# Performance work log

Hardware: AMD Instinct MI355X
Metric: run time of the kernel (lower is better)

Reference implementation:

```python
import jax, jax.numpy as jnp
import numpy as np

# Model dims (see init_kwargs): embed_dim=64, heads=8, d_k = n_wires = 8
V, D, H, NQ, L, FFN = 32000, 64, 8, 8, 2, 128
B, S = 16, 1024
LAT, H1, H2, NC = 32, 128, 64, 10
INV_SQRT_DK = 1.0 / float(np.sqrt(NQ))
LN_EPS = 1e-5


def _pos_encoding(s, d):
    pos = jnp.arange(s, dtype=jnp.float32)[:, None]
    div = jnp.exp(jnp.arange(0, d, 2, dtype=jnp.float32) * (-np.log(10000.0) / d))
    pe = jnp.zeros((s, d), dtype=jnp.float32)
    pe = pe.at[:, 0::2].set(jnp.sin(pos * div))
    pe = pe.at[:, 1::2].set(jnp.cos(pos * div))
    return pe


def _layernorm(x, g, b):
    mu = jnp.mean(x, axis=-1, keepdims=True)
    var = jnp.mean(jnp.square(x - mu), axis=-1, keepdims=True)
    return (x - mu) * jax.lax.rsqrt(var + LN_EPS) * g + b


def _quantum_heads(x, theta):
    # Analytic simulation of the per-head 8-qubit VQC:
    #   RX(x_i) RX(theta_i) on wire i, CNOT ring (0->1..6->7, 7->0), measure Z.
    # Heisenberg picture: <Z_j> = prod_{i=0..j} cos(x_i+theta_i) for j>=1,
    # <Z_0> = prod_{i=1..7} cos(x_i+theta_i).
    b, s, _ = x.shape
    a = x.reshape(b, s, H, NQ) + theta            # [B,S,H,NQ]
    c = jnp.cos(a)
    cp = jnp.cumprod(c, axis=-1)
    z0 = jnp.prod(c[..., 1:], axis=-1, keepdims=True)
    return jnp.concatenate([z0, cp[..., 1:]], axis=-1)  # [B,S,H,NQ]


def _quantum_attention(x, theta, combine_W):
    qkv = _quantum_heads(x, theta)                 # [B,S,H,dk]
    q = qkv.transpose(0, 2, 1, 3)                  # [B,H,S,dk]
    scores = jnp.einsum('bhqd,bhkd->bhqk', q, q) * INV_SQRT_DK
    p = jax.nn.softmax(scores, axis=-1)
    out = jnp.einsum('bhqk,bhkd->bhqd', p, q)
    out = out.transpose(0, 2, 1, 3).reshape(x.shape[0], x.shape[1], D)
    return out @ combine_W.T                       # no bias (use_bias=False)


def _quantum_ffn(x, theta, W1, b1, W2, b2):
    # FFN QLayer: RX(x_i) then RY(theta_i), no entanglement -> <Z_i> = cos(theta_i)*cos(x_i)
    # GeneralEncoder only reads the first NQ features of each token.
    z = jnp.cos(x[..., :NQ]) * jnp.cos(theta)      # [B,S,NQ]
    h = jax.nn.relu(z @ W1.T + b1)                 # linear1 then ReLU
    return h @ W2.T + b2                           # linear2


def _forward(tokens, emb_table, attn_theta, combine_W, ln1_g, ln1_b, ln2_g, ln2_b,
             ffn_theta, ffn_W1, ffn_b1, ffn_W2, ffn_b2,
             enc_W1, enc_b1, enc_W2, enc_b2, enc_W3, enc_b3,
             dec_W1, dec_b1, dec_W2, dec_b2, dec_W3, dec_b3, cls_W, cls_b):
    x = emb_table[tokens] + _pos_encoding(tokens.shape[1], D)  # embed + positional
    for l in range(L):  # fixed small number of structurally distinct blocks
        a = _quantum_attention(x, attn_theta[l], combine_W[l])
        x = _layernorm(x + a, ln1_g[l], ln1_b[l])
        f = _quantum_ffn(x, ffn_theta[l], ffn_W1[l], ffn_b1[l], ffn_W2[l], ffn_b2[l])
        x = _layernorm(x + f, ln2_g[l], ln2_b[l])
    pooled = jnp.mean(x, axis=1)                   # [B,D]
    # AutoencoderQuantumNet.forward = decode(encode(x)) (quantum_ffn unused there)
    h = jax.nn.relu(pooled @ enc_W1.T + enc_b1)
    h = jax.nn.relu(h @ enc_W2.T + enc_b2)
    lat = h @ enc_W3.T + enc_b3
    h = jax.nn.relu(lat @ dec_W1.T + dec_b1)
    h = jax.nn.relu(h @ dec_W2.T + dec_b2)
    rec = h @ dec_W3.T + dec_b3                    # [B,D]
    return rec @ cls_W.T + cls_b                   # [B,NC]


def setup_inputs() -> dict:
    key = jax.random.key(0)
    ks = list(jax.random.split(key, 32))
    it = iter(ks)
    def nrm(shape, scale=0.05):
        return (jax.random.normal(next(it), shape) * scale).astype(jnp.float32)
    return {
        'tokens': jax.random.randint(next(it), (B, S), 0, V),
        'emb_table': nrm((V, D), 0.02),
        'attn_theta': nrm((L, NQ), 0.1),
        'combine_W': nrm((L, D, D)),
        'ln1_g': jnp.ones((L, D), jnp.float32), 'ln1_b': jnp.zeros((L, D), jnp.float32),
        'ln2_g': jnp.ones((L, D), jnp.float32), 'ln2_b': jnp.zeros((L, D), jnp.float32),
        'ffn_theta': nrm((L, NQ), 0.1),
        'ffn_W1': nrm((L, FFN, NQ)), 'ffn_b1': jnp.zeros((L, FFN), jnp.float32),
        'ffn_W2': nrm((L, D, FFN)), 'ffn_b2': jnp.zeros((L, D), jnp.float32),
        'enc_W1': nrm((H1, D)), 'enc_b1': jnp.zeros((H1,), jnp.float32),
        'enc_W2': nrm((H2, H1)), 'enc_b2': jnp.zeros((H2,), jnp.float32),
        'enc_W3': nrm((LAT, H2)), 'enc_b3': jnp.zeros((LAT,), jnp.float32),
        'dec_W1': nrm((H2, LAT)), 'dec_b1': jnp.zeros((H2,), jnp.float32),
        'dec_W2': nrm((H1, H2)), 'dec_b2': jnp.zeros((H1,), jnp.float32),
        'dec_W3': nrm((D, H1)), 'dec_b3': jnp.zeros((D,), jnp.float32),
        'cls_W': nrm((NC, D)), 'cls_b': jnp.zeros((NC,), jnp.float32),
    }


def reference(tokens, emb_table, attn_theta, combine_W, ln1_g, ln1_b, ln2_g, ln2_b,
              ffn_theta, ffn_W1, ffn_b1, ffn_W2, ffn_b2,
              enc_W1, enc_b1, enc_W2, enc_b2, enc_W3, enc_b3,
              dec_W1, dec_b1, dec_W2, dec_b2, dec_W3, dec_b3, cls_W, cls_b):
    return _forward(tokens, emb_table, attn_theta, combine_W, ln1_g, ln1_b, ln2_g, ln2_b,
                    ffn_theta, ffn_W1, ffn_b1, ffn_W2, ffn_b2,
                    enc_W1, enc_b1, enc_W2, enc_b2, enc_W3, enc_b3,
                    dec_W1, dec_b1, dec_W2, dec_b2, dec_W3, dec_b3, cls_W, cls_b)
```

## Files before the change

kernel.cpp:

```cpp
#include <hip/hip_runtime.h>
#include <math.h>

typedef _Float16 h2 __attribute__((ext_vector_type(2)));
typedef __fp16 hh4 __attribute__((ext_vector_type(4)));
typedef float f4 __attribute__((ext_vector_type(4)));

#define Bsz 16
#define Ssz 1024
#define TOKENS (Bsz * Ssz)
#define Dd 64
#define Hh 8
#define QTTS 520

#if __has_builtin(__builtin_amdgcn_exp2f)
  #define EXPFN(x) __builtin_amdgcn_exp2f(x)
  #define SQRT_PRESCALE 0.7141921f
#else
  #define EXPFN(x) __expf(x)
  #define SQRT_PRESCALE 0.5946036f
#endif

#if __has_builtin(__builtin_amdgcn_mfma_f32_16x16x16_f16)
  #define MFMA16(a, b, c) __builtin_amdgcn_mfma_f32_16x16x16_f16(a, b, c, 0, 0, 0)
#else
  #define MFMA16(a, b, c) __builtin_amdgcn_mfma_f32_16x16x16f16(a, b, c, 0, 0, 0)
#endif

__device__ __forceinline__ h2 pkrtz(float a, float b) {
#if __has_builtin(__builtin_amdgcn_cvt_pkrtz)
  return __builtin_bit_cast(h2, __builtin_amdgcn_cvt_pkrtz(a, b));
#else
  h2 r; r.x = (_Float16)a; r.y = (_Float16)b; return r;
#endif
}
__device__ __forceinline__ unsigned int as_u32(h2 v) {
  return __builtin_bit_cast(unsigned int, v);
}
__device__ __forceinline__ hh4 bc4(uint2 u) {
  return __builtin_bit_cast(hh4, u);
}

__device__ __forceinline__ void qheads(const float* __restrict__ xp,
                                       const float* th, float* o) {
  float4 v0 = *(const float4*)(xp);
  float4 v1 = *(const float4*)(xp + 4);
  float c0 = __cosf(v0.x + th[0]), c1 = __cosf(v0.y + th[1]);
  float c2 = __cosf(v0.z + th[2]), c3 = __cosf(v0.w + th[3]);
  float c4 = __cosf(v1.x + th[4]), c5 = __cosf(v1.y + th[5]);
  float c6 = __cosf(v1.z + th[6]), c7 = __cosf(v1.w + th[7]);
  float cp = c0;
  cp *= c1; o[1] = cp; cp *= c2; o[2] = cp; cp *= c3; o[3] = cp;
  cp *= c4; o[4] = cp; cp *= c5; o[5] = cp; cp *= c6; o[6] = cp;
  cp *= c7; o[7] = cp;
  o[0] = c1 * c2 * c3 * c4 * c5 * c6 * c7;
}

__global__ __launch_bounds__(256) void embed_kernel(
    const int* __restrict__ tokens, const float* __restrict__ emb,
    float* __restrict__ x) {
  int gid = blockIdx.x * 256 + threadIdx.x;
  if (gid >= TOKENS * 32) return;
  int d2 = gid & 31;
  int ts = gid >> 5;
  int s  = ts & (Ssz - 1);
  int tok = tokens[ts];
  float freq = __expf((float)(2 * d2) * (-0.14391156831f));
  float ang = (float)s * freq;
  float sn, cs;
  __sincosf(ang, &sn, &cs);
  float2 e2 = *(const float2*)&emb[(size_t)tok * Dd + 2 * d2];
  float2 r;
  r.x = e2.x + sn;
  r.y = e2.y + cs;
  *(float2*)&x[(size_t)ts * Dd + 2 * d2] = r;
}

__global__ __launch_bounds__(256, 4) void attn_kernel(
    const float* __restrict__ x, const float* __restrict__ theta,
    float* __restrict__ o_out, float* __restrict__ ps_out) {
  __shared__ unsigned int qrs[Ssz * 4 + 2];
  __shared__ unsigned int qtt[9 * QTTS];
  int blk = blockIdx.x;
  int bh = blk >> 3, split = blk & 7;
  int b = bh >> 3, h = bh & 7;
  int t = threadIdx.x;

  float th[8];
#pragma unroll
  for (int i = 0; i < 8; i++) th[i] = theta[i];

  const float* xb = x + (size_t)b * Ssz * Dd + h * 8;

#pragma unroll
  for (int i = 0; i < 4; i += 2) {
    int k0 = t * 4 + i;
    float oa[8], ob[8];
    qheads(xb + (size_t)k0 * Dd, th, oa);
    qheads(xb + (size_t)(k0 + 1) * Dd, th, ob);
    uint4 wa, wb;
    wa.x = as_u32(pkrtz(oa[0] * SQRT_PRESCALE, oa[1] * SQRT_PRESCALE));
    wa.y = as_u32(pkrtz(oa[2] * SQRT_PRESCALE, oa[3] * SQRT_PRESCALE));
    wa.z = as_u32(pkrtz(oa[4] * SQRT_PRESCALE, oa[5] * SQRT_PRESCALE));
    wa.w = as_u32(pkrtz(oa[6] * SQRT_PRESCALE, oa[7] * SQRT_PRESCALE));
    wb.x = as_u32(pkrtz(ob[0] * SQRT_PRESCALE, ob[1] * SQRT_PRESCALE));
    wb.y = as_u32(pkrtz(ob[2] * SQRT_PRESCALE, ob[3] * SQRT_PRESCALE));
    wb.z = as_u32(pkrtz(ob[4] * SQRT_PRESCALE, ob[5] * SQRT_PRESCALE));
    wb.w = as_u32(pkrtz(ob[6] * SQRT_PRESCALE, ob[7] * SQRT_PRESCALE));
    *(uint4*)&qrs[k0 * 4] = wa;
    *(uint4*)&qrs[(k0 + 1) * 4] = wb;
#pragma unroll
    for (int d = 0; d < 8; d++)
      qtt[d * QTTS + (k0 >> 1)] = as_u32(pkrtz(oa[d], ob[d]));
  }
  for (int j = 8 * QTTS + t; j < 9 * QTTS; j += 256) qtt[j] = 0x3C003C00u;
  if (t == 0) { qrs[Ssz * 4] = 0; qrs[Ssz * 4 + 1] = 0; }
  __syncthreads();

  int l = t & 63, w = t >> 6;
  int g = l >> 4, rr = l & 15;
  int rt0 = split * 8 + w * 2;
  int rowA = rt0 * 16 + rr;
  int rowB = rowA + 16;
  uint2 z2; z2.x = 0; z2.y = 0;
  uint2 buA = (g < 2) ? *(const uint2*)&qrs[rowA * 4 + 2 * g] : z2;
  uint2 buB = (g < 2) ? *(const uint2*)&qrs[rowB * 4 + 2 * g] : z2;
  hh4 BrA = bc4(buA), BrB = bc4(buB);
  int aoff  = (g < 2) ? (rr * 4 + 2 * g) : (Ssz * 4);
  int astep = (g < 2) ? 64 : 0;
  int qrow  = (rr >= 8) ? 8 : rr;
  int qoff  = qrow * QTTS + 2 * g;
  f4 zf = {0.f, 0.f, 0.f, 0.f};
  f4 accA0 = zf, accB0 = zf, accA1 = zf, accB1 = zf;

#pragma unroll 4
  for (int kt = 0; kt < 64; kt += 2) {
    {
      uint2 au = *(const uint2*)&qrs[aoff + kt * astep];
      hh4 Ak = bc4(au);
      f4 sA = MFMA16(Ak, BrA, zf);
      f4 sB = MFMA16(Ak, BrB, zf);
      float pA0 = EXPFN(sA.x), pA1 = EXPFN(sA.y), pA2 = EXPFN(sA.z), pA3 = EXPFN(sA.w);
      float pB0 = EXPFN(sB.x), pB1 = EXPFN(sB.y), pB2 = EXPFN(sB.z), pB3 = EXPFN(sB.w);
      uint2 pbA, pbB;
      pbA.x = as_u32(pkrtz(pA0, pA1)); pbA.y = as_u32(pkrtz(pA2, pA3));
      pbB.x = as_u32(pkrtz(pB0, pB1)); pbB.y = as_u32(pkrtz(pB2, pB3));
      uint2 qt = *(const uint2*)&qtt[qoff + kt * 8];
      hh4 Aq = bc4(qt);
      accA0 = MFMA16(Aq, bc4(pbA), accA0);
      accB0 = MFMA16(Aq, bc4(pbB), accB0);
    }
    {
      uint2 au = *(const uint2*)&qrs[aoff + (kt + 1) * astep];
      hh4 Ak = bc4(au);
      f4 sA = MFMA16(Ak, BrA, zf);
      f4 sB = MFMA16(Ak, BrB, zf);
      float pA0 = EXPFN(sA.x), pA1 = EXPFN(sA.y), pA2 = EXPFN(sA.z), pA3 = EXPFN(sA.w);
      float pB0 = EXPFN(sB.x), pB1 = EXPFN(sB.y), pB2 = EXPFN(sB.z), pB3 = EXPFN(sB.w);
      uint2 pbA, pbB;
      pbA.x = as_u32(pkrtz(pA0, pA1)); pbA.y = as_u32(pkrtz(pA2, pA3));
      pbB.x = as_u32(pkrtz(pB0, pB1)); pbB.y = as_u32(pkrtz(pB2, pB3));
      uint2 qt = *(const uint2*)&qtt[qoff + (kt + 1) * 8];
      hh4 Aq = bc4(qt);
      accA1 = MFMA16(Aq, bc4(pbA), accA1);
      accB1 = MFMA16(Aq, bc4(pbB), accB1);
    }
  }
  f4 accA = accA0 + accA1;
  f4 accB = accB0 + accB1;

  size_t tokA = (size_t)b * Ssz + rowA;
  size_t tokB = (size_t)b * Ssz + rowB;
  if (g < 2) {
    *(f4*)&o_out[tokA * 64 + h * 8 + 4 * g] = accA;
    *(f4*)&o_out[tokB * 64 + h * 8 + 4 * g] = accB;
  } else if (g == 2) {
    ps_out[tokA * 8 + h] = accA.x;
    ps_out[tokB * 8 + h] = accB.x;
  }
}

__global__ __launch_bounds__(64) void tail_kernel(
    float* __restrict__ x, const float* __restrict__ o_out,
    const float* __restrict__ ps_out, const float* __restrict__ Wc,
    const float* __restrict__ g1, const float* __restrict__ bb1,
    const float* __restrict__ g2, const float* __restrict__ bb2,
    const float* __restrict__ fth,
    const float* __restrict__ W1, const float* __restrict__ fb1,
    const float* __restrict__ W2, const float* __restrict__ fb2,
    float* __restrict__ partial, int do_partial) {
  __shared__ float xbuf[16][68];
  int l = threadIdx.x & 63;
  int g = l >> 4, c = l & 15;
  int tok0 = blockIdx.x * 16;
  f4 zf = {0.f, 0.f, 0.f, 0.f};

  {
    hh4 Bf[4][4];
#pragma unroll
    for (int dc = 0; dc < 4; dc++)
#pragma unroll
      for (int kc = 0; kc < 4; kc++) {
        float4 wv = *(const float4*)&Wc[(size_t)(dc * 16 + c) * 64 + kc * 16 + 4 * g];
        uint2 u; u.x = as_u32(pkrtz(wv.x, wv.y)); u.y = as_u32(pkrtz(wv.z, wv.w));
        Bf[kc][dc] = bc4(u);
      }
    int tka = tok0 + c;
    hh4 Af[4];
#pragma unroll
    for (int kc = 0; kc < 4; kc++) {
      float4 o4 = *(const float4*)&o_out[(size_t)tka * 64 + kc * 16 + 4 * g];
      float inv = 1.0f / ps_out[(size_t)tka * 8 + kc * 2 + (g >> 1)];
      uint2 u;
      u.x = as_u32(pkrtz(o4.x * inv, o4.y * inv));
      u.y = as_u32(pkrtz(o4.z * inv, o4.w * inv));
      Af[kc] = bc4(u);
    }
    float yy[4][4];
#pragma unroll
    for (int dc = 0; dc < 4; dc++) {
      f4 acc = zf;
#pragma unroll
      for (int kc = 0; kc < 4; kc++) acc = MFMA16(Af[kc], Bf[kc][dc], acc);
      yy[dc][0] = acc.x; yy[dc][1] = acc.y; yy[dc][2] = acc.z; yy[dc][3] = acc.w;
    }
    float g1v[4], b1v[4];
#pragma unroll
    for (int dc = 0; dc < 4; dc++) { g1v[dc] = g1[dc * 16 + c]; b1v[dc] = bb1[dc * 16 + c]; }
#pragma unroll
    for (int r = 0; r < 4; r++) {
      int tok = tok0 + 4 * g + r;
      float rv0 = x[(size_t)tok * 64 + c]      + yy[0][r];
      float rv1 = x[(size_t)tok * 64 + 16 + c] + yy[1][r];
      float rv2 = x[(size_t)tok * 64 + 32 + c] + yy[2][r];
      float rv3 = x[(size_t)tok * 64 + 48 + c] + yy[3][r];
      float s = (rv0 + rv1) + (rv2 + rv3);
      s += __shfl_xor(s, 1, 64); s += __shfl_xor(s, 2, 64);
      s += __shfl_xor(s, 4, 64); s += __shfl_xor(s, 8, 64);
      float mu = s * (1.f / 64.f);
      float t0 = rv0 - mu, t1 = rv1 - mu, t2 = rv2 - mu, t3 = rv3 - mu;
      float q = (t0 * t0 + t1 * t1) + (t2 * t2 + t3 * t3);
      q += __shfl_xor(q, 1, 64); q += __shfl_xor(q, 2, 64);
      q += __shfl_xor(q, 4, 64); q += __shfl_xor(q, 8, 64);
      float inv = rsqrtf(q * (1.f / 64.f) + 1e-5f);
      int tk = 4 * g + r;
      xbuf[tk][c]      = t0 * inv * g1v[0] + b1v[0];
      xbuf[tk][16 + c] = t1 * inv * g1v[1] + b1v[1];
      xbuf[tk][32 + c] = t2 * inv * g1v[2] + b1v[2];
      xbuf[tk][48 + c] = t3 * inv * g1v[3] + b1v[3];
    }
  }

  float4 x4[4];
#pragma unroll
  for (int dc = 0; dc < 4; dc++)
    x4[dc] = *(const float4*)&xbuf[c][dc * 16 + 4 * g];

  uint2 uz; uz.x = 0; uz.y = 0;
  if (g < 2) {
    float4 thv = *(const float4*)&fth[4 * g];
    float z0 = __cosf(x4[0].x) * __cosf(thv.x);
    float z1 = __cosf(x4[0].y) * __cosf(thv.y);
    float z2 = __cosf(x4[0].z) * __cosf(thv.z);
    float z3 = __cosf(x4[0].w) * __cosf(thv.w);
    uz.x = as_u32(pkrtz(z0, z1)); uz.y = as_u32(pkrtz(z2, z3));
  }
  hh4 Bz = bc4(uz);

  hh4 Bh[8];
#pragma unroll
  for (int jc = 0; jc < 8; jc++) {
    uint2 uw; uw.x = 0; uw.y = 0;
    if (g < 2) {
      float4 wv = *(const float4*)&W1[(size_t)(jc * 16 + c) * 8 + 4 * g];
      uw.x = as_u32(pkrtz(wv.x, wv.y)); uw.y = as_u32(pkrtz(wv.z, wv.w));
    }
    f4 d1 = MFMA16(bc4(uw), Bz, zf);
    float4 b1v = *(const float4*)&fb1[jc * 16 + 4 * g];
    float h0 = fmaxf(d1.x + b1v.x, 0.f);
    float h1 = fmaxf(d1.y + b1v.y, 0.f);
    float h2 = fmaxf(d1.z + b1v.z, 0.f);
    float h3 = fmaxf(d1.w + b1v.w, 0.f);
    uint2 uh;
    uh.x = as_u32(pkrtz(h0, h1)); uh.y = as_u32(pkrtz(h2, h3));
    Bh[jc] = bc4(uh);
  }

  float ff[4][4];
#pragma unroll
  for (int dc = 0; dc < 4; dc++) {
    f4 acc = zf;
#pragma unroll
    for (int kc = 0; kc < 8; kc++) {
      float4 wv = *(const float4*)&W2[(size_t)(dc * 16 + c) * 128 + kc * 16 + 4 * g];
      uint2 uw;
      uw.x = as_u32(pkrtz(wv.x, wv.y)); uw.y = as_u32(pkrtz(wv.z, wv.w));
      acc = MFMA16(bc4(uw), Bh[kc], acc);
    }
    ff[dc][0] = acc.x; ff[dc][1] = acc.y; ff[dc][2] = acc.z; ff[dc][3] = acc.w;
  }

  float r2[4][4];
  float s = 0.f;
#pragma unroll
  for (int dc = 0; dc < 4; dc++) {
    float4 b2v = *(const float4*)&fb2[dc * 16 + 4 * g];
    r2[dc][0] = x4[dc].x + ff[dc][0] + b2v.x;
    r2[dc][1] = x4[dc].y + ff[dc][1] + b2v.y;
    r2[dc][2] = x4[dc].z + ff[dc][2] + b2v.z;
    r2[dc][3] = x4[dc].w + ff[dc][3] + b2v.w;
    s += (r2[dc][0] + r2[dc][1]) + (r2[dc][2] + r2[dc][3]);
  }
  s += __shfl_xor(s, 16, 64); s += __shfl_xor(s, 32, 64);
  float mu = s * (1.f / 64.f);
  float q = 0.f;
#pragma unroll
  for (int dc = 0; dc < 4; dc++) {
#pragma unroll
    for (int r = 0; r < 4; r++) { r2[dc][r] -= mu; q += r2[dc][r] * r2[dc][r]; }
  }
  q += __shfl_xor(q, 16, 64); q += __shfl_xor(q, 32, 64);
  float inv = rsqrtf(q * (1.f / 64.f) + 1e-5f);

  float xo[4][4];
#pragma unroll
  for (int dc = 0; dc < 4; dc++) {
    float4 gv = *(const float4*)&g2[dc * 16 + 4 * g];
    float4 bv = *(const float4*)&bb2[dc * 16 + 4 * g];
    xo[dc][0] = r2[dc][0] * inv * gv.x + bv.x;
    xo[dc][1] = r2[dc][1] * inv * gv.y + bv.y;
    xo[dc][2] = r2[dc][2] * inv * gv.z + bv.z;
    xo[dc][3] = r2[dc][3] * inv * gv.w + bv.w;
    float4 o4;
    o4.x = xo[dc][0]; o4.y = xo[dc][1]; o4.z = xo[dc][2]; o4.w = xo[dc][3];
    *(float4*)&x[(size_t)(tok0 + c) * 64 + dc * 16 + 4 * g] = o4;
  }

  if (do_partial) {
#pragma unroll
    for (int dc = 0; dc < 4; dc++)
#pragma unroll
      for (int r = 0; r < 4; r++) {
        float p = xo[dc][r];
        p += __shfl_xor(p, 1, 64); p += __shfl_xor(p, 2, 64);
        p += __shfl_xor(p, 4, 64); p += __shfl_xor(p, 8, 64);
        xo[dc][r] = p;
      }
    if (c == 0) {
#pragma unroll
      for (int dc = 0; dc < 4; dc++) {
        float4 o4;
        o4.x = xo[dc][0]; o4.y = xo[dc][1]; o4.z = xo[dc][2]; o4.w = xo[dc][3];
        *(float4*)&partial[(size_t)blockIdx.x * 64 + dc * 16 + 4 * g] = o4;
      }
    }
  }
}

__global__ __launch_bounds__(128) void head_kernel(
    const float* __restrict__ partial,
    const float* eW1, const float* eb1, const float* eW2, const float* eb2,
    const float* eW3, const float* eb3, const float* dW1, const float* db1v,
    const float* dW2, const float* db2v, const float* dW3, const float* db3v,
    const float* cW, const float* cb, float* __restrict__ out) {
  __shared__ float bufP[64];
  __shared__ float bufA[128];
  __shared__ float bufB[128];
  int b = blockIdx.x, t = threadIdx.x;
  if (t < 64) {
    float s = 0.f;
    for (int c = 0; c < 64; ++c) s += partial[(size_t)(b * 64 + c) * 64 + t];
    bufP[t] = s * (1.f / 1024.f);
  }
  __syncthreads();
  {
    float v = eb1[t];
    for (int d = 0; d < 64; d++) v = fmaf(bufP[d], eW1[t * 64 + d], v);
    bufA[t] = fmaxf(v, 0.f);
  }
  __syncthreads();
  if (t < 64) {
    float v = eb2[t];
    for (int j = 0; j < 128; j++) v = fmaf(bufA[j], eW2[t * 128 + j], v);
    bufB[t] = fmaxf(v, 0.f);
  }
  __syncthreads();
  if (t < 32) {
    float v = eb3[t];
    for (int d = 0; d < 64; d++) v = fmaf(bufB[d], eW3[t * 64 + d], v);
    bufA[t] = v;
  }
  __syncthreads();
  if (t < 64) {
    float v = db1v[t];
    for (int k = 0; k < 32; k++) v = fmaf(bufA[k], dW1[t * 32 + k], v);
    bufB[t] = fmaxf(v, 0.f);
  }
  __syncthreads();
  {
    float v = db2v[t];
    for (int k = 0; k < 64; k++) v = fmaf(bufB[k], dW2[t * 64 + k], v);
    bufA[t] = fmaxf(v, 0.f);
  }
  __syncthreads();
  if (t < 64) {
    float v = db3v[t];
    for (int j = 0; j < 128; j++) v = fmaf(bufA[j], dW3[t * 128 + j], v);
    bufB[t] = v;
  }
  __syncthreads();
  if (t < 10) {
    float v = cb[t];
    for (int d = 0; d < 64; d++) v = fmaf(bufB[d], cW[t * 64 + d], v);
    out[b * 10 + t] = v;
  }
}

extern "C" void kernel_launch(void* const* d_in, const int* in_sizes, int n_in,
                              void* d_out, int out_size, void* d_ws, size_t ws_size,
                              hipStream_t stream) {
  const int*   tokens     = (const int*)d_in[0];
  const float* emb        = (const float*)d_in[1];
  const float* attn_theta = (const float*)d_in[2];
  const float* combine_W  = (const float*)d_in[3];
  const float* ln1_g      = (const float*)d_in[4];
  const float* ln1_b      = (const float*)d_in[5];
  const float* ln2_g      = (const float*)d_in[6];
  const float* ln2_b      = (const float*)d_in[7];
  const float* ffn_theta  = (const float*)d_in[8];
  const float* ffn_W1     = (const float*)d_in[9];
  const float* ffn_b1     = (const float*)d_in[10];
  const float* ffn_W2     = (const float*)d_in[11];
  const float* ffn_b2     = (const float*)d_in[12];
  const float* enc_W1 = (const float*)d_in[13]; const float* enc_b1 = (const float*)d_in[14];
  const float* enc_W2 = (const float*)d_in[15]; const float* enc_b2 = (const float*)d_in[16];
  const float* enc_W3 = (const float*)d_in[17]; const float* enc_b3 = (const float*)d_in[18];
  const float* dec_W1 = (const float*)d_in[19]; const float* dec_b1 = (const float*)d_in[20];
  const float* dec_W2 = (const float*)d_in[21]; const float* dec_b2 = (const float*)d_in[22];
  const float* dec_W3 = (const float*)d_in[23]; const float* dec_b3 = (const float*)d_in[24];
  const float* cls_W  = (const float*)d_in[25]; const float* cls_b  = (const float*)d_in[26];

  float* x       = (float*)d_ws;
  float* o_out   = x + (size_t)TOKENS * 64;
  float* ps_out  = o_out + (size_t)TOKENS * 64;
  float* partial = ps_out + (size_t)TOKENS * 8;
  float* out     = (float*)d_out;

  embed_kernel<<<(TOKENS * 32 + 255) / 256, 256, 0, stream>>>(tokens, emb, x);
  for (int l = 0; l < 2; ++l) {
    attn_kernel<<<128 * 8, 256, 0, stream>>>(x, attn_theta + l * 8, o_out, ps_out);
    tail_kernel<<<TOKENS / 16, 64, 0, stream>>>(
        x, o_out, ps_out, combine_W + l * 4096,
        ln1_g + l * 64, ln1_b + l * 64, ln2_g + l * 64, ln2_b + l * 64,
        ffn_theta + l * 8, ffn_W1 + l * 1024, ffn_b1 + l * 128,
        ffn_W2 + l * 8192, ffn_b2 + l * 64, partial, (l == 1) ? 1 : 0);
  }
  head_kernel<<<16, 128, 0, stream>>>(partial, enc_W1, enc_b1, enc_W2, enc_b2,
                                      enc_W3, enc_b3, dec_W1, dec_b1, dec_W2,
                                      dec_b2, dec_W3, dec_b3, cls_W, cls_b, out);
}
```

Before: 89.91 us.

## Fuse embedding and positional encoding into first-layer attention kernel

Removes the separate embedding kernel. The first attention launch, a template instance with EMBED=1, now gathers token embeddings and adds the sinusoidal positional encoding directly. The split-0 block writes the resulting x for the later tail kernel. Head preprocessing is restructured to one token per iteration with 16-bit stores into the transposed LDS buffer, and the main loop hoists its LDS loads ahead of the MFMA chain. This saves a launch and one write/read pass over x, at the cost of all 8 split blocks redundantly recomputing the gather and sincos, plus narrower LDS stores.

```diff
diff --git a/kernel.cpp b/kernel.cpp
--- a/kernel.cpp
+++ b/kernel.cpp
@@ -40,14 +40,11 @@
   return __builtin_bit_cast(hh4, u);
 }
 
-__device__ __forceinline__ void qheads(const float* __restrict__ xp,
-                                       const float* th, float* o) {
-  float4 v0 = *(const float4*)(xp);
-  float4 v1 = *(const float4*)(xp + 4);
-  float c0 = __cosf(v0.x + th[0]), c1 = __cosf(v0.y + th[1]);
-  float c2 = __cosf(v0.z + th[2]), c3 = __cosf(v0.w + th[3]);
-  float c4 = __cosf(v1.x + th[4]), c5 = __cosf(v1.y + th[5]);
-  float c6 = __cosf(v1.z + th[6]), c7 = __cosf(v1.w + th[7]);
+__device__ __forceinline__ void qheads_v(const float* xa, const float* th, float* o) {
+  float c0 = __cosf(xa[0] + th[0]), c1 = __cosf(xa[1] + th[1]);
+  float c2 = __cosf(xa[2] + th[2]), c3 = __cosf(xa[3] + th[3]);
+  float c4 = __cosf(xa[4] + th[4]), c5 = __cosf(xa[5] + th[5]);
+  float c6 = __cosf(xa[6] + th[6]), c7 = __cosf(xa[7] + th[7]);
   float cp = c0;
   cp *= c1; o[1] = cp; cp *= c2; o[2] = cp; cp *= c3; o[3] = cp;
   cp *= c4; o[4] = cp; cp *= c5; o[5] = cp; cp *= c6; o[6] = cp;
@@ -55,28 +52,11 @@
   o[0] = c1 * c2 * c3 * c4 * c5 * c6 * c7;
 }
 
-__global__ __launch_bounds__(256) void embed_kernel(
+template <int EMBED>
+__global__ __launch_bounds__(256, 4) void attn_kernel(
+    const float* __restrict__ x, float* __restrict__ xw,
     const int* __restrict__ tokens, const float* __restrict__ emb,
-    float* __restrict__ x) {
-  int gid = blockIdx.x * 256 + threadIdx.x;
-  if (gid >= TOKENS * 32) return;
-  int d2 = gid & 31;
-  int ts = gid >> 5;
-  int s  = ts & (Ssz - 1);
-  int tok = tokens[ts];
-  float freq = __expf((float)(2 * d2) * (-0.14391156831f));
-  float ang = (float)s * freq;
-  float sn, cs;
-  __sincosf(ang, &sn, &cs);
-  float2 e2 = *(const float2*)&emb[(size_t)tok * Dd + 2 * d2];
-  float2 r;
-  r.x = e2.x + sn;
-  r.y = e2.y + cs;
-  *(float2*)&x[(size_t)ts * Dd + 2 * d2] = r;
-}
-
-__global__ __launch_bounds__(256, 4) void attn_kernel(
-    const float* __restrict__ x, const float* __restrict__ theta,
+    const float* __restrict__ theta,
     float* __restrict__ o_out, float* __restrict__ ps_out) {
   __shared__ unsigned int qrs[Ssz * 4 + 2];
   __shared__ unsigned int qtt[9 * QTTS];
@@ -89,28 +69,56 @@
 #pragma unroll
   for (int i = 0; i < 8; i++) th[i] = theta[i];
 
+  float frq[4];
+  if (EMBED) {
+#pragma unroll
+    for (int j = 0; j < 4; j++)
+      frq[j] = __expf((float)(2 * (h * 4 + j)) * (-0.14391156831f));
+  }
+
   const float* xb = x + (size_t)b * Ssz * Dd + h * 8;
 
 #pragma unroll
-  for (int i = 0; i < 4; i += 2) {
+  for (int i = 0; i < 4; i++) {
     int k0 = t * 4 + i;
-    float oa[8], ob[8];
-    qheads(xb + (size_t)k0 * Dd, th, oa);
-    qheads(xb + (size_t)(k0 + 1) * Dd, th, ob);
-    uint4 wa, wb;
+    float xa[8];
+    if (EMBED) {
+      int tok = tokens[b * Ssz + k0];
+      float4 e0 = *(const float4*)&emb[(size_t)tok * Dd + h * 8];
+      float4 e1 = *(const float4*)&emb[(size_t)tok * Dd + h * 8 + 4];
+      float sn, cs;
+      __sincosf((float)k0 * frq[0], &sn, &cs); xa[0] = e0.x + sn; xa[1] = e0.y + cs;
+      __sincosf((float)k0 * frq[1], &sn, &cs); xa[2] = e0.z + sn; xa[3] = e0.w + cs;
+      __sincosf((float)k0 * frq[2], &sn, &cs); xa[4] = e1.x + sn; xa[5] = e1.y + cs;
+      __sincosf((float)k0 * frq[3], &sn, &cs); xa[6] = e1.z + sn; xa[7] = e1.w + cs;
+      if (split == 0) {
+        float4 w0, w1;
+        w0.x = xa[0]; w0.y = xa[1]; w0.z = xa[2]; w0.w = xa[3];
+        w1.x = xa[4]; w1.y = xa[5]; w1.z = xa[6]; w1.w = xa[7];
+        *(float4*)&xw[((size_t)b * Ssz + k0) * Dd + h * 8] = w0;
+        *(float4*)&xw[((size_t)b * Ssz + k0) * Dd + h * 8 + 4] = w1;
+      }
+    } else {
+      float4 v0 = *(const float4*)(xb + (size_t)k0 * Dd);
+      float4 v1 = *(const float4*)(xb + (size_t)k0 * Dd + 4);
+      xa[0] = v0.x; xa[1] = v0.y; xa[2] = v0.z; xa[3] = v0.w;
+      xa[4] = v1.x; xa[5] = v1.y; xa[6] = v1.z; xa[7] = v1.w;
+    }
+    float oa[8];
+    qheads_v(xa, th, oa);
+    uint4 wa;
     wa.x = as_u32(pkrtz(oa[0] * SQRT_PRESCALE, oa[1] * SQRT_PRESCALE));
     wa.y = as_u32(pkrtz(oa[2] * SQRT_PRESCALE, oa[3] * SQRT_PRESCALE));
     wa.z = as_u32(pkrtz(oa[4] * SQRT_PRESCALE, oa[5] * SQRT_PRESCALE));
     wa.w = as_u32(pkrtz(oa[6] * SQRT_PRESCALE, oa[7] * SQRT_PRESCALE));
-    wb.x = as_u32(pkrtz(ob[0] * SQRT_PRESCALE, ob[1] * SQRT_PRESCALE));
-    wb.y = as_u32(pkrtz(ob[2] * SQRT_PRESCALE, ob[3] * SQRT_PRESCALE));
-    wb.z = as_u32(pkrtz(ob[4] * SQRT_PRESCALE, ob[5] * SQRT_PRESCALE));
-    wb.w = as_u32(pkrtz(ob[6] * SQRT_PRESCALE, ob[7] * SQRT_PRESCALE));
     *(uint4*)&qrs[k0 * 4] = wa;
-    *(uint4*)&qrs[(k0 + 1) * 4] = wb;
-#pragma unroll
-    for (int d = 0; d < 8; d++)
-      qtt[d * QTTS + (k0 >> 1)] = as_u32(pkrtz(oa[d], ob[d]));
+    if (i & 1) {
+    }
+#pragma unroll
+    for (int d = 0; d < 8; d++) {
+      unsigned short hv = (unsigned short)(as_u32(pkrtz(oa[d], oa[d])) & 0xFFFFu);
+      ((unsigned short*)&qtt[d * QTTS + (k0 >> 1)])[k0 & 1] = hv;
+    }
   }
   for (int j = 8 * QTTS + t; j < 9 * QTTS; j += 256) qtt[j] = 0x3C003C00u;
   if (t == 0) { qrs[Ssz * 4] = 0; qrs[Ssz * 4 + 1] = 0; }
@@ -134,9 +142,12 @@
 
 #pragma unroll 4
   for (int kt = 0; kt < 64; kt += 2) {
+    uint2 au0 = *(const uint2*)&qrs[aoff + kt * astep];
+    uint2 au1 = *(const uint2*)&qrs[aoff + (kt + 1) * astep];
+    uint2 qt0 = *(const uint2*)&qtt[qoff + kt * 8];
+    uint2 qt1 = *(const uint2*)&qtt[qoff + (kt + 1) * 8];
     {
-      uint2 au = *(const uint2*)&qrs[aoff + kt * astep];
-      hh4 Ak = bc4(au);
+      hh4 Ak = bc4(au0);
       f4 sA = MFMA16(Ak, BrA, zf);
       f4 sB = MFMA16(Ak, BrB, zf);
       float pA0 = EXPFN(sA.x), pA1 = EXPFN(sA.y), pA2 = EXPFN(sA.z), pA3 = EXPFN(sA.w);
@@ -144,14 +155,12 @@
       uint2 pbA, pbB;
       pbA.x = as_u32(pkrtz(pA0, pA1)); pbA.y = as_u32(pkrtz(pA2, pA3));
       pbB.x = as_u32(pkrtz(pB0, pB1)); pbB.y = as_u32(pkrtz(pB2, pB3));
-      uint2 qt = *(const uint2*)&qtt[qoff + kt * 8];
-      hh4 Aq = bc4(qt);
+      hh4 Aq = bc4(qt0);
       accA0 = MFMA16(Aq, bc4(pbA), accA0);
       accB0 = MFMA16(Aq, bc4(pbB), accB0);
     }
     {
-      uint2 au = *(const uint2*)&qrs[aoff + (kt + 1) * astep];
-      hh4 Ak = bc4(au);
+      hh4 Ak = bc4(au1);
       f4 sA = MFMA16(Ak, BrA, zf);
       f4 sB = MFMA16(Ak, BrB, zf);
       float pA0 = EXPFN(sA.x), pA1 = EXPFN(sA.y), pA2 = EXPFN(sA.z), pA3 = EXPFN(sA.w);
@@ -159,8 +168,7 @@
       uint2 pbA, pbB;
       pbA.x = as_u32(pkrtz(pA0, pA1)); pbA.y = as_u32(pkrtz(pA2, pA3));
       pbB.x = as_u32(pkrtz(pB0, pB1)); pbB.y = as_u32(pkrtz(pB2, pB3));
-      uint2 qt = *(const uint2*)&qtt[qoff + (kt + 1) * 8];
-      hh4 Aq = bc4(qt);
+      hh4 Aq = bc4(qt1);
       accA1 = MFMA16(Aq, bc4(pbA), accA1);
       accB1 = MFMA16(Aq, bc4(pbB), accB1);
     }
@@ -445,15 +453,19 @@
   float* partial = ps_out + (size_t)TOKENS * 8;
   float* out     = (float*)d_out;
 
-  embed_kernel<<<(TOKENS * 32 + 255) / 256, 256, 0, stream>>>(tokens, emb, x);
-  for (int l = 0; l < 2; ++l) {
-    attn_kernel<<<128 * 8, 256, 0, stream>>>(x, attn_theta + l * 8, o_out, ps_out);
-    tail_kernel<<<TOKENS / 16, 64, 0, stream>>>(
-        x, o_out, ps_out, combine_W + l * 4096,
-        ln1_g + l * 64, ln1_b + l * 64, ln2_g + l * 64, ln2_b + l * 64,
-        ffn_theta + l * 8, ffn_W1 + l * 1024, ffn_b1 + l * 128,
-        ffn_W2 + l * 8192, ffn_b2 + l * 64, partial, (l == 1) ? 1 : 0);
-  }
+  attn_kernel<1><<<128 * 8, 256, 0, stream>>>(x, x, tokens, emb,
+                                              attn_theta, o_out, ps_out);
+  tail_kernel<<<TOKENS / 16, 64, 0, stream>>>(
+      x, o_out, ps_out, combine_W,
+      ln1_g, ln1_b, ln2_g, ln2_b,
+      ffn_theta, ffn_W1, ffn_b1, ffn_W2, ffn_b2, partial, 0);
+  attn_kernel<0><<<128 * 8, 256, 0, stream>>>(x, x, tokens, emb,
+                                              attn_theta + 8, o_out, ps_out);
+  tail_kernel<<<TOKENS / 16, 64, 0, stream>>>(
+      x, o_out, ps_out, combine_W + 4096,
+      ln1_g + 64, ln1_b + 64, ln2_g + 64, ln2_b + 64,
+      ffn_theta + 8, ffn_W1 + 1024, ffn_b1 + 128,
+      ffn_W2 + 8192, ffn_b2 + 64, partial, 1);
   head_kernel<<<16, 128, 0, stream>>>(partial, enc_W1, enc_b1, enc_W2, enc_b2,
                                       enc_W3, enc_b3, dec_W1, dec_b1, dec_W2,
                                       dec_b2, dec_W3, dec_b3, cls_W, cls_b, out);
```

After: 90.51 us. About the same (+0.7%).
